# Kernel tuning notes

Hardware: AMD Instinct MI355X
Metric: run time of the kernel (lower is better)

Reference implementation:

```python
import jax, jax.numpy as jnp
import numpy as np

N = 200_000   # fluid particles
DEG = 40      # avg neighbors (2D Wendland support)
E = N * DEG   # edges
SUPPORT = 0.05


def setup_inputs() -> dict:
    key = jax.random.key(0)
    ks = jax.random.split(key, 10)
    i = jnp.sort(jax.random.randint(ks[0], (E,), 0, N))          # target particle per edge
    j = jax.random.randint(ks[1], (E,), 0, N)                    # neighbor particle per edge
    ri = jax.random.uniform(ks[2], (N, 2), dtype=jnp.float32)    # positions (unused in math)
    rj = ri
    dx = SUPPORT * 0.4
    Vi = (0.5 + jax.random.uniform(ks[3], (N,), dtype=jnp.float32)) * dx * dx  # volumes
    Vj = Vi
    d = jax.random.normal(ks[4], (E, 2), dtype=jnp.float32)
    distances = d / jnp.linalg.norm(d, axis=1, keepdims=True)    # unit directions x_ij/|x_ij|
    radialDistances = jax.random.uniform(ks[5], (E,), dtype=jnp.float32)  # q = r/h in [0,1]
    rhoi = 1000.0 * (0.99 + 0.02 * jax.random.uniform(ks[6], (N,), dtype=jnp.float32))
    rhoj = rhoi
    p = 1000.0 * jax.random.normal(ks[7], (N,), dtype=jnp.float32)  # EOS pressure
    return {
        "i": i, "j": j, "ri": ri, "rj": rj, "Vi": Vi, "Vj": Vj,
        "distances": distances, "radialDistances": radialDistances,
        "support": jnp.float32(SUPPORT), "numParticles": N,
        "eps": jnp.float32(SUPPORT * SUPPORT * 0.1),
        "rhoi": rhoi, "rhoj": rhoj, "pi": p, "pj": p,
    }


def _kernel_gradient(q, directions, h):
    # 2D Wendland C2: dW/dq = -20 q (1-q)^3 * (7/pi) / h^3, applied along unit direction
    C = 7.0 / np.pi
    mag = -20.0 * q * (1.0 - q) ** 3 * C / (h ** 3)
    return directions * mag[:, None]  # [E, 2]


def reference(i, j, ri, rj, Vi, Vj, distances, radialDistances, support,
              numParticles, eps, rhoi, rhoj, pi, pj):
    gradW = _kernel_gradient(radialDistances, distances, support)      # [E, 2]
    pij = pi[i] + pj[j]                                                # [E]
    term = (pij * Vj[j])[:, None] * gradW                              # [E, 2]
    acc = jax.ops.segment_sum(term, i, num_segments=numParticles)     # [N, 2]
    return -1.0 / rhoi[:, None] * acc
```

## Files before the change

### kernel.cpp

```cpp
#include <hip/hip_runtime.h>


constexpr int CHUNK = 8;

__global__ void pack_pv(const float* __restrict__ p,
                        const float* __restrict__ V,
                        float2* __restrict__ pv, int N)
{
    int n = blockIdx.x * blockDim.x + threadIdx.x;
    if (n < N) pv[n] = make_float2(p[n], V[n]);
}

__global__ __launch_bounds__(256) void edge_kernel(
    const int*    __restrict__ ei,
    const int*    __restrict__ ej,
    const float*  __restrict__ dirs,
    const float*  __restrict__ qarr,
    const float*  __restrict__ support,
    const float*  __restrict__ p_i,
    const float2* __restrict__ pv,
    float*        __restrict__ acc,
    long long E)
{
    long long t    = blockIdx.x * (long long)blockDim.x + threadIdx.x;
    long long base = t * CHUNK;
    const int lane = threadIdx.x & 63;

    int   cur = -1;
    float ax = 0.0f, ay = 0.0f;

    if (base < E) {
        const float h    = support[0];
        const float coef = -20.0f * (7.0f / 3.14159265358979323846f) / (h * h * h);

        int   ii[CHUNK], jj[CHUNK];
        float qq[CHUNK], dxv[CHUNK], dyv[CHUNK];
        int   nk;

        if (base + CHUNK <= E) {
            const int4*   pi4 = (const int4*)  (ei   + base);
            const int4*   pj4 = (const int4*)  (ej   + base);
            const float4* pq4 = (const float4*)(qarr + base);
            const float4* pd4 = (const float4*)(dirs + 2 * base);
            int4   ia = pi4[0], ib = pi4[1];
            int4   ja = pj4[0], jb = pj4[1];
            float4 qa = pq4[0], qb = pq4[1];
            float4 d0 = pd4[0], d1 = pd4[1], d2 = pd4[2], d3 = pd4[3];
            ii[0]=ia.x; ii[1]=ia.y; ii[2]=ia.z; ii[3]=ia.w;
            ii[4]=ib.x; ii[5]=ib.y; ii[6]=ib.z; ii[7]=ib.w;
            jj[0]=ja.x; jj[1]=ja.y; jj[2]=ja.z; jj[3]=ja.w;
            jj[4]=jb.x; jj[5]=jb.y; jj[6]=jb.z; jj[7]=jb.w;
            qq[0]=qa.x; qq[1]=qa.y; qq[2]=qa.z; qq[3]=qa.w;
            qq[4]=qb.x; qq[5]=qb.y; qq[6]=qb.z; qq[7]=qb.w;
            dxv[0]=d0.x; dyv[0]=d0.y; dxv[1]=d0.z; dyv[1]=d0.w;
            dxv[2]=d1.x; dyv[2]=d1.y; dxv[3]=d1.z; dyv[3]=d1.w;
            dxv[4]=d2.x; dyv[4]=d2.y; dxv[5]=d2.z; dyv[5]=d2.w;
            dxv[6]=d3.x; dyv[6]=d3.y; dxv[7]=d3.z; dyv[7]=d3.w;
            nk = CHUNK;
        } else {
            nk = (int)(E - base);
            #pragma unroll
            for (int k = 0; k < CHUNK; ++k) {
                if (k < nk) {
                    ii[k]  = ei[base + k];
                    jj[k]  = ej[base + k];
                    qq[k]  = qarr[base + k];
                    dxv[k] = dirs[2 * (base + k)];
                    dyv[k] = dirs[2 * (base + k) + 1];
                } else { ii[k] = 0; jj[k] = 0; qq[k] = 0.0f; dxv[k] = 0.0f; dyv[k] = 0.0f; }
            }
        }

        float2 pvv[CHUNK];
        float  piv[CHUNK];
        #pragma unroll
        for (int k = 0; k < CHUNK; ++k) pvv[k] = pv[jj[k]];
        #pragma unroll
        for (int k = 0; k < CHUNK; ++k) piv[k] = p_i[ii[k]];

        float w[CHUNK];
        #pragma unroll
        for (int k = 0; k < CHUNK; ++k) {
            float om = 1.0f - qq[k];
            w[k] = (piv[k] + pvv[k].x) * pvv[k].y * (coef * qq[k] * om * om * om);
        }

        cur = ii[0];
        #pragma unroll
        for (int k = 0; k < CHUNK; ++k) {
            if (k < nk) {
                if (ii[k] != cur) {
                    atomicAdd(&acc[2 * cur],     ax);
                    atomicAdd(&acc[2 * cur + 1], ay);
                    cur = ii[k];
                    ax = 0.0f; ay = 0.0f;
                }
                ax += w[k] * dxv[k];
                ay += w[k] * dyv[k];
            }
        }
    }

    #pragma unroll
    for (int d = 1; d < 64; d <<= 1) {
        int   oc  = __shfl_up(cur, d);
        float oax = __shfl_up(ax,  d);
        float oay = __shfl_up(ay,  d);
        if (lane >= d && oc == cur) { ax += oax; ay += oay; }
    }
    int nxt = __shfl_down(cur, 1);
    if (cur >= 0 && (lane == 63 || nxt != cur)) {
        atomicAdd(&acc[2 * cur],     ax);
        atomicAdd(&acc[2 * cur + 1], ay);
    }
}

__global__ void finalize_kernel(float2* __restrict__ out,
                                const float* __restrict__ rhoi,
                                int N)
{
    int n = blockIdx.x * blockDim.x + threadIdx.x;
    if (n < N) {
        float2 a  = out[n];
        float  sc = -1.0f / rhoi[n];
        out[n] = make_float2(a.x * sc, a.y * sc);
    }
}

extern "C" void kernel_launch(void* const* d_in, const int* in_sizes, int n_in,
                              void* d_out, int out_size, void* d_ws, size_t ws_size,
                              hipStream_t stream)
{
    const int*   ei      = (const int*)  d_in[0];
    const int*   ej      = (const int*)  d_in[1];
    const float* Vj      = (const float*)d_in[5];
    const float* dirs    = (const float*)d_in[6];
    const float* qarr    = (const float*)d_in[7];
    const float* support = (const float*)d_in[8];
    const float* rhoi    = (const float*)d_in[11];
    const float* p_i     = (const float*)d_in[13];
    const float* p_j     = (const float*)d_in[14];

    const long long E = in_sizes[0];
    const int       N = in_sizes[11];

    float* out = (float*)d_out;
    hipMemsetAsync(out, 0, (size_t)N * 2 * sizeof(float), stream);

    const int block = 256;
    float2* pv = (float2*)d_ws;
    pack_pv<<<(N + block - 1) / block, block, 0, stream>>>(p_j, Vj, pv, N);

    const long long nthreads = (E + CHUNK - 1) / CHUNK;
    const int grid = (int)((nthreads + block - 1) / block);
    edge_kernel<<<grid, block, 0, stream>>>(ei, ej, dirs, qarr, support,
                                            p_i, pv, out, E);

    finalize_kernel<<<(N + block - 1) / block, block, 0, stream>>>((float2*)out, rhoi, N);
}
```

Baseline: 70.67 us.

## Fuse memset and finalize into prep kernel, scale atomics by -1/rho in edge kernel

Merges the output zeroing memset and the pack kernel into one prep kernel that also precomputes -1/rho per particle, and removes the finalize pass by scaling each partial sum before its atomicAdd. This cuts two launches and a full read-write pass over the output. It also reorders the loads so the gathered p/V reads issue before the streaming q/direction loads, and adds an occupancy hint of 8 blocks per CU to launch_bounds. In exchange, the edge kernel does an extra gather of -1/rho for every atomic flush.

```diff
diff --git a/kernel.cpp b/kernel.cpp
--- a/kernel.cpp
+++ b/kernel.cpp
@@ -3,15 +3,24 @@
 
 constexpr int CHUNK = 8;
 
-__global__ void pack_pv(const float* __restrict__ p,
-                        const float* __restrict__ V,
-                        float2* __restrict__ pv, int N)
+__global__ __launch_bounds__(256) void prep_kernel(
+    const float* __restrict__ p,
+    const float* __restrict__ V,
+    const float* __restrict__ rho,
+    float2*      __restrict__ pv,
+    float*       __restrict__ nr,
+    float2*      __restrict__ out,
+    int N)
 {
     int n = blockIdx.x * blockDim.x + threadIdx.x;
-    if (n < N) pv[n] = make_float2(p[n], V[n]);
+    if (n < N) {
+        pv[n]  = make_float2(p[n], V[n]);
+        nr[n]  = -1.0f / rho[n];
+        out[n] = make_float2(0.0f, 0.0f);
+    }
 }
 
-__global__ __launch_bounds__(256) void edge_kernel(
+__global__ __launch_bounds__(256, 8) void edge_kernel(
     const int*    __restrict__ ei,
     const int*    __restrict__ ej,
     const float*  __restrict__ dirs,
@@ -19,6 +28,7 @@
     const float*  __restrict__ support,
     const float*  __restrict__ p_i,
     const float2* __restrict__ pv,
+    const float*  __restrict__ nr,
     float*        __restrict__ acc,
     long long E)
 {
@@ -33,41 +43,25 @@
         const float h    = support[0];
         const float coef = -20.0f * (7.0f / 3.14159265358979323846f) / (h * h * h);
 
-        int   ii[CHUNK], jj[CHUNK];
-        float qq[CHUNK], dxv[CHUNK], dyv[CHUNK];
-        int   nk;
+        int ii[CHUNK], jj[CHUNK];
+        int nk;
 
         if (base + CHUNK <= E) {
-            const int4*   pi4 = (const int4*)  (ei   + base);
-            const int4*   pj4 = (const int4*)  (ej   + base);
-            const float4* pq4 = (const float4*)(qarr + base);
-            const float4* pd4 = (const float4*)(dirs + 2 * base);
-            int4   ia = pi4[0], ib = pi4[1];
-            int4   ja = pj4[0], jb = pj4[1];
-            float4 qa = pq4[0], qb = pq4[1];
-            float4 d0 = pd4[0], d1 = pd4[1], d2 = pd4[2], d3 = pd4[3];
+            const int4* pi4 = (const int4*)(ei + base);
+            const int4* pj4 = (const int4*)(ej + base);
+            int4 ia = pi4[0], ib = pi4[1];
+            int4 ja = pj4[0], jb = pj4[1];
             ii[0]=ia.x; ii[1]=ia.y; ii[2]=ia.z; ii[3]=ia.w;
             ii[4]=ib.x; ii[5]=ib.y; ii[6]=ib.z; ii[7]=ib.w;
             jj[0]=ja.x; jj[1]=ja.y; jj[2]=ja.z; jj[3]=ja.w;
             jj[4]=jb.x; jj[5]=jb.y; jj[6]=jb.z; jj[7]=jb.w;
-            qq[0]=qa.x; qq[1]=qa.y; qq[2]=qa.z; qq[3]=qa.w;
-            qq[4]=qb.x; qq[5]=qb.y; qq[6]=qb.z; qq[7]=qb.w;
-            dxv[0]=d0.x; dyv[0]=d0.y; dxv[1]=d0.z; dyv[1]=d0.w;
-            dxv[2]=d1.x; dyv[2]=d1.y; dxv[3]=d1.z; dyv[3]=d1.w;
-            dxv[4]=d2.x; dyv[4]=d2.y; dxv[5]=d2.z; dyv[5]=d2.w;
-            dxv[6]=d3.x; dyv[6]=d3.y; dxv[7]=d3.z; dyv[7]=d3.w;
             nk = CHUNK;
         } else {
             nk = (int)(E - base);
             #pragma unroll
             for (int k = 0; k < CHUNK; ++k) {
-                if (k < nk) {
-                    ii[k]  = ei[base + k];
-                    jj[k]  = ej[base + k];
-                    qq[k]  = qarr[base + k];
-                    dxv[k] = dirs[2 * (base + k)];
-                    dyv[k] = dirs[2 * (base + k) + 1];
-                } else { ii[k] = 0; jj[k] = 0; qq[k] = 0.0f; dxv[k] = 0.0f; dyv[k] = 0.0f; }
+                ii[k] = (k < nk) ? ei[base + k] : 0;
+                jj[k] = (k < nk) ? ej[base + k] : 0;
             }
         }
 
@@ -77,6 +71,27 @@
         for (int k = 0; k < CHUNK; ++k) pvv[k] = pv[jj[k]];
         #pragma unroll
         for (int k = 0; k < CHUNK; ++k) piv[k] = p_i[ii[k]];
+
+        float qq[CHUNK], dxv[CHUNK], dyv[CHUNK];
+        if (base + CHUNK <= E) {
+            const float4* pq4 = (const float4*)(qarr + base);
+            const float4* pd4 = (const float4*)(dirs + 2 * base);
+            float4 qa = pq4[0], qb = pq4[1];
+            float4 d0 = pd4[0], d1 = pd4[1], d2 = pd4[2], d3 = pd4[3];
+            qq[0]=qa.x; qq[1]=qa.y; qq[2]=qa.z; qq[3]=qa.w;
+            qq[4]=qb.x; qq[5]=qb.y; qq[6]=qb.z; qq[7]=qb.w;
+            dxv[0]=d0.x; dyv[0]=d0.y; dxv[1]=d0.z; dyv[1]=d0.w;
+            dxv[2]=d1.x; dyv[2]=d1.y; dxv[3]=d1.z; dyv[3]=d1.w;
+            dxv[4]=d2.x; dyv[4]=d2.y; dxv[5]=d2.z; dyv[5]=d2.w;
+            dxv[6]=d3.x; dyv[6]=d3.y; dxv[7]=d3.z; dyv[7]=d3.w;
+        } else {
+            #pragma unroll
+            for (int k = 0; k < CHUNK; ++k) {
+                qq[k]  = (k < nk) ? qarr[base + k]           : 0.0f;
+                dxv[k] = (k < nk) ? dirs[2 * (base + k)]     : 0.0f;
+                dyv[k] = (k < nk) ? dirs[2 * (base + k) + 1] : 0.0f;
+            }
+        }
 
         float w[CHUNK];
         #pragma unroll
@@ -90,8 +105,9 @@
         for (int k = 0; k < CHUNK; ++k) {
             if (k < nk) {
                 if (ii[k] != cur) {
-                    atomicAdd(&acc[2 * cur],     ax);
-                    atomicAdd(&acc[2 * cur + 1], ay);
+                    float s = nr[cur];
+                    atomicAdd(&acc[2 * cur],     ax * s);
+                    atomicAdd(&acc[2 * cur + 1], ay * s);
                     cur = ii[k];
                     ax = 0.0f; ay = 0.0f;
                 }
@@ -110,20 +126,9 @@
     }
     int nxt = __shfl_down(cur, 1);
     if (cur >= 0 && (lane == 63 || nxt != cur)) {
-        atomicAdd(&acc[2 * cur],     ax);
-        atomicAdd(&acc[2 * cur + 1], ay);
-    }
-}
-
-__global__ void finalize_kernel(float2* __restrict__ out,
-                                const float* __restrict__ rhoi,
-                                int N)
-{
-    int n = blockIdx.x * blockDim.x + threadIdx.x;
-    if (n < N) {
-        float2 a  = out[n];
-        float  sc = -1.0f / rhoi[n];
-        out[n] = make_float2(a.x * sc, a.y * sc);
+        float s = nr[cur];
+        atomicAdd(&acc[2 * cur],     ax * s);
+        atomicAdd(&acc[2 * cur + 1], ay * s);
     }
 }
 
@@ -144,17 +149,16 @@
     const long long E = in_sizes[0];
     const int       N = in_sizes[11];
 
-    float* out = (float*)d_out;
-    hipMemsetAsync(out, 0, (size_t)N * 2 * sizeof(float), stream);
+    float2* pv = (float2*)d_ws;
+    float*  nr = (float*)((char*)d_ws + (size_t)N * sizeof(float2));
 
     const int block = 256;
-    float2* pv = (float2*)d_ws;
-    pack_pv<<<(N + block - 1) / block, block, 0, stream>>>(p_j, Vj, pv, N);
+
+    prep_kernel<<<(N + block - 1) / block, block, 0, stream>>>(
+        p_j, Vj, rhoi, pv, nr, (float2*)d_out, N);
 
     const long long nthreads = (E + CHUNK - 1) / CHUNK;
     const int grid = (int)((nthreads + block - 1) / block);
-    edge_kernel<<<grid, block, 0, stream>>>(ei, ej, dirs, qarr, support,
-                                            p_i, pv, out, E);
-
-    finalize_kernel<<<(N + block - 1) / block, block, 0, stream>>>((float2*)out, rhoi, N);
+    edge_kernel<<<grid, block, 0, stream>>>(
+        ei, ej, dirs, qarr, support, p_i, pv, nr, (float*)d_out, E);
 }
```

Result: slower. 78.24 us (+10.7%).

## Persistent grid-stride edge kernel with software-pipelined index and gather prefetch

Applied to the files above, without the earlier changes.

The edge kernel becomes a persistent grid-stride loop over a fixed grid of 1024 blocks. Each iteration prefetches the next chunk's i/j indices, then issues the next chunk's gathers and streaming loads while the current chunk's wave-level segmented reduction and atomics run. The output memset is folded into the pack kernel, which removes one launch. In exchange the kernel holds more live registers, and a fixed grid may underfill or overfill the GPU.

```diff
diff --git a/kernel.cpp b/kernel.cpp
--- a/kernel.cpp
+++ b/kernel.cpp
@@ -1,17 +1,26 @@
 #include <hip/hip_runtime.h>
 
 
-constexpr int CHUNK = 8;
-
-__global__ void pack_pv(const float* __restrict__ p,
-                        const float* __restrict__ V,
-                        float2* __restrict__ pv, int N)
+constexpr int   CHUNK = 8;
+constexpr int   BLOCK = 256;
+constexpr int   GRID  = 1024;
+constexpr float PI_F  = 3.14159265358979323846f;
+
+__global__ __launch_bounds__(BLOCK) void prep_kernel(
+    const float* __restrict__ p,
+    const float* __restrict__ V,
+    float2*      __restrict__ pv,
+    float2*      __restrict__ out,
+    int N)
 {
     int n = blockIdx.x * blockDim.x + threadIdx.x;
-    if (n < N) pv[n] = make_float2(p[n], V[n]);
-}
-
-__global__ __launch_bounds__(256) void edge_kernel(
+    if (n < N) {
+        pv[n]  = make_float2(p[n], V[n]);
+        out[n] = make_float2(0.0f, 0.0f);
+    }
+}
+
+__global__ __launch_bounds__(BLOCK) void edge_kernel(
     const int*    __restrict__ ei,
     const int*    __restrict__ ej,
     const float*  __restrict__ dirs,
@@ -22,61 +31,86 @@
     float*        __restrict__ acc,
     long long E)
 {
-    long long t    = blockIdx.x * (long long)blockDim.x + threadIdx.x;
-    long long base = t * CHUNK;
+    const long long T   = (long long)GRID * BLOCK;
+    const long long NC  = (E + CHUNK - 1) / CHUNK;
+    long long c   = blockIdx.x * (long long)blockDim.x + threadIdx.x;
     const int lane = threadIdx.x & 63;
-
-    int   cur = -1;
-    float ax = 0.0f, ay = 0.0f;
-
-    if (base < E) {
-        const float h    = support[0];
-        const float coef = -20.0f * (7.0f / 3.14159265358979323846f) / (h * h * h);
-
-        int   ii[CHUNK], jj[CHUNK];
-        float qq[CHUNK], dxv[CHUNK], dyv[CHUNK];
-        int   nk;
-
-        if (base + CHUNK <= E) {
-            const int4*   pi4 = (const int4*)  (ei   + base);
-            const int4*   pj4 = (const int4*)  (ej   + base);
-            const float4* pq4 = (const float4*)(qarr + base);
-            const float4* pd4 = (const float4*)(dirs + 2 * base);
-            int4   ia = pi4[0], ib = pi4[1];
-            int4   ja = pj4[0], jb = pj4[1];
-            float4 qa = pq4[0], qb = pq4[1];
-            float4 d0 = pd4[0], d1 = pd4[1], d2 = pd4[2], d3 = pd4[3];
-            ii[0]=ia.x; ii[1]=ia.y; ii[2]=ia.z; ii[3]=ia.w;
-            ii[4]=ib.x; ii[5]=ib.y; ii[6]=ib.z; ii[7]=ib.w;
-            jj[0]=ja.x; jj[1]=ja.y; jj[2]=ja.z; jj[3]=ja.w;
-            jj[4]=jb.x; jj[5]=jb.y; jj[6]=jb.z; jj[7]=jb.w;
-            qq[0]=qa.x; qq[1]=qa.y; qq[2]=qa.z; qq[3]=qa.w;
-            qq[4]=qb.x; qq[5]=qb.y; qq[6]=qb.z; qq[7]=qb.w;
-            dxv[0]=d0.x; dyv[0]=d0.y; dxv[1]=d0.z; dyv[1]=d0.w;
-            dxv[2]=d1.x; dyv[2]=d1.y; dxv[3]=d1.z; dyv[3]=d1.w;
-            dxv[4]=d2.x; dyv[4]=d2.y; dxv[5]=d2.z; dyv[5]=d2.w;
-            dxv[6]=d3.x; dyv[6]=d3.y; dxv[7]=d3.z; dyv[7]=d3.w;
-            nk = CHUNK;
-        } else {
-            nk = (int)(E - base);
-            #pragma unroll
-            for (int k = 0; k < CHUNK; ++k) {
-                if (k < nk) {
-                    ii[k]  = ei[base + k];
-                    jj[k]  = ej[base + k];
-                    qq[k]  = qarr[base + k];
-                    dxv[k] = dirs[2 * (base + k)];
-                    dyv[k] = dirs[2 * (base + k) + 1];
-                } else { ii[k] = 0; jj[k] = 0; qq[k] = 0.0f; dxv[k] = 0.0f; dyv[k] = 0.0f; }
-            }
-        }
-
-        float2 pvv[CHUNK];
-        float  piv[CHUNK];
-        #pragma unroll
-        for (int k = 0; k < CHUNK; ++k) pvv[k] = pv[jj[k]];
-        #pragma unroll
-        for (int k = 0; k < CHUNK; ++k) piv[k] = p_i[ii[k]];
+    long long wfc = c - lane;
+
+    if (wfc >= NC) return;
+
+    const float h    = support[0];
+    const float coef = -20.0f * (7.0f / PI_F) / (h * h * h);
+
+    int    iiA[CHUNK], jjA[CHUNK];
+    int    iiB[CHUNK], jjB[CHUNK];
+    float2 pvv[CHUNK];
+    float  piv[CHUNK], qq[CHUNK], dxv[CHUNK], dyv[CHUNK];
+
+#define LOAD_IDX(cc, ii, jj)                                                   \
+    do {                                                                       \
+        long long b_ = (cc) * CHUNK;                                           \
+        if ((cc) < NC && b_ + CHUNK <= E) {                                    \
+            const int4* pi4_ = (const int4*)(ei + b_);                         \
+            const int4* pj4_ = (const int4*)(ej + b_);                         \
+            int4 ia_ = pi4_[0], ib_ = pi4_[1];                                 \
+            int4 ja_ = pj4_[0], jb_ = pj4_[1];                                 \
+            ii[0]=ia_.x; ii[1]=ia_.y; ii[2]=ia_.z; ii[3]=ia_.w;                \
+            ii[4]=ib_.x; ii[5]=ib_.y; ii[6]=ib_.z; ii[7]=ib_.w;                \
+            jj[0]=ja_.x; jj[1]=ja_.y; jj[2]=ja_.z; jj[3]=ja_.w;                \
+            jj[4]=jb_.x; jj[5]=jb_.y; jj[6]=jb_.z; jj[7]=jb_.w;                \
+        } else {                                                               \
+            _Pragma("unroll")                                                  \
+            for (int k_ = 0; k_ < CHUNK; ++k_) {                               \
+                long long e_ = b_ + k_;                                        \
+                bool ok_ = ((cc) < NC) && (e_ < E);                            \
+                ii[k_] = ok_ ? ei[e_] : -1;                                    \
+                jj[k_] = ok_ ? ej[e_] : 0;                                     \
+            }                                                                  \
+        }                                                                      \
+    } while (0)
+
+#define LOAD_GS(cc, ii, jj)                                                    \
+    do {                                                                       \
+        long long b_ = (cc) * CHUNK;                                           \
+        _Pragma("unroll")                                                      \
+        for (int k_ = 0; k_ < CHUNK; ++k_) pvv[k_] = pv[jj[k_]];               \
+        _Pragma("unroll")                                                      \
+        for (int k_ = 0; k_ < CHUNK; ++k_) {                                   \
+            int i_ = ii[k_] < 0 ? 0 : ii[k_];                                  \
+            piv[k_] = p_i[i_];                                                 \
+        }                                                                      \
+        if ((cc) < NC && b_ + CHUNK <= E) {                                    \
+            const float4* pq4_ = (const float4*)(qarr + b_);                   \
+            const float4* pd4_ = (const float4*)(dirs + 2 * b_);               \
+            float4 qa_ = pq4_[0], qb_ = pq4_[1];                               \
+            float4 d0_ = pd4_[0], d1_ = pd4_[1], d2_ = pd4_[2], d3_ = pd4_[3]; \
+            qq[0]=qa_.x; qq[1]=qa_.y; qq[2]=qa_.z; qq[3]=qa_.w;                \
+            qq[4]=qb_.x; qq[5]=qb_.y; qq[6]=qb_.z; qq[7]=qb_.w;                \
+            dxv[0]=d0_.x; dyv[0]=d0_.y; dxv[1]=d0_.z; dyv[1]=d0_.w;            \
+            dxv[2]=d1_.x; dyv[2]=d1_.y; dxv[3]=d1_.z; dyv[3]=d1_.w;            \
+            dxv[4]=d2_.x; dyv[4]=d2_.y; dxv[5]=d2_.z; dyv[5]=d2_.w;            \
+            dxv[6]=d3_.x; dyv[6]=d3_.y; dxv[7]=d3_.z; dyv[7]=d3_.w;            \
+        } else {                                                               \
+            _Pragma("unroll")                                                  \
+            for (int k_ = 0; k_ < CHUNK; ++k_) {                               \
+                long long e_ = b_ + k_;                                        \
+                bool ok_ = ((cc) < NC) && (e_ < E);                            \
+                qq[k_]  = ok_ ? qarr[e_]           : 0.0f;                     \
+                dxv[k_] = ok_ ? dirs[2 * e_]       : 0.0f;                     \
+                dyv[k_] = ok_ ? dirs[2 * e_ + 1]   : 0.0f;                     \
+            }                                                                  \
+        }                                                                      \
+    } while (0)
+
+    LOAD_IDX(c, iiA, jjA);
+    LOAD_GS(c, iiA, jjA);
+
+    for (;;) {
+        long long cn = c + T;
+        bool have_next = (wfc + T) < NC;
+
+        if (have_next) LOAD_IDX(cn, iiB, jjB);
 
         float w[CHUNK];
         #pragma unroll
@@ -85,39 +119,52 @@
             w[k] = (piv[k] + pvv[k].x) * pvv[k].y * (coef * qq[k] * om * om * om);
         }
 
-        cur = ii[0];
+        int   cur = iiA[0];
+        float ax = 0.0f, ay = 0.0f;
         #pragma unroll
         for (int k = 0; k < CHUNK; ++k) {
-            if (k < nk) {
-                if (ii[k] != cur) {
+            if (iiA[k] != cur) {
+                if (cur >= 0) {
                     atomicAdd(&acc[2 * cur],     ax);
                     atomicAdd(&acc[2 * cur + 1], ay);
-                    cur = ii[k];
-                    ax = 0.0f; ay = 0.0f;
                 }
-                ax += w[k] * dxv[k];
-                ay += w[k] * dyv[k];
+                cur = iiA[k];
+                ax = 0.0f; ay = 0.0f;
             }
-        }
+            ax += w[k] * dxv[k];
+            ay += w[k] * dyv[k];
+        }
+
+        if (have_next) LOAD_GS(cn, iiB, jjB);
+
+        #pragma unroll
+        for (int d = 1; d < 64; d <<= 1) {
+            int   oc  = __shfl_up(cur, d);
+            float oax = __shfl_up(ax,  d);
+            float oay = __shfl_up(ay,  d);
+            if (lane >= d && oc == cur) { ax += oax; ay += oay; }
+        }
+        int nxt = __shfl_down(cur, 1);
+        if (cur >= 0 && (lane == 63 || nxt != cur)) {
+            atomicAdd(&acc[2 * cur],     ax);
+            atomicAdd(&acc[2 * cur + 1], ay);
+        }
+
+        if (!have_next) break;
+        #pragma unroll
+        for (int k = 0; k < CHUNK; ++k) { iiA[k] = iiB[k]; jjA[k] = jjB[k]; }
+        c = cn;
+        wfc += T;
     }
 
-    #pragma unroll
-    for (int d = 1; d < 64; d <<= 1) {
-        int   oc  = __shfl_up(cur, d);
-        float oax = __shfl_up(ax,  d);
-        float oay = __shfl_up(ay,  d);
-        if (lane >= d && oc == cur) { ax += oax; ay += oay; }
-    }
-    int nxt = __shfl_down(cur, 1);
-    if (cur >= 0 && (lane == 63 || nxt != cur)) {
-        atomicAdd(&acc[2 * cur],     ax);
-        atomicAdd(&acc[2 * cur + 1], ay);
-    }
-}
-
-__global__ void finalize_kernel(float2* __restrict__ out,
-                                const float* __restrict__ rhoi,
-                                int N)
+#undef LOAD_IDX
+#undef LOAD_GS
+}
+
+__global__ __launch_bounds__(BLOCK) void finalize_kernel(
+    float2* __restrict__ out,
+    const float* __restrict__ rhoi,
+    int N)
 {
     int n = blockIdx.x * blockDim.x + threadIdx.x;
     if (n < N) {
@@ -144,17 +191,14 @@
     const long long E = in_sizes[0];
     const int       N = in_sizes[11];
 
-    float* out = (float*)d_out;
-    hipMemsetAsync(out, 0, (size_t)N * 2 * sizeof(float), stream);
-
-    const int block = 256;
     float2* pv = (float2*)d_ws;
-    pack_pv<<<(N + block - 1) / block, block, 0, stream>>>(p_j, Vj, pv, N);
-
-    const long long nthreads = (E + CHUNK - 1) / CHUNK;
-    const int grid = (int)((nthreads + block - 1) / block);
-    edge_kernel<<<grid, block, 0, stream>>>(ei, ej, dirs, qarr, support,
-                                            p_i, pv, out, E);
-
-    finalize_kernel<<<(N + block - 1) / block, block, 0, stream>>>((float2*)out, rhoi, N);
-}
+
+    prep_kernel<<<(N + BLOCK - 1) / BLOCK, BLOCK, 0, stream>>>(
+        p_j, Vj, pv, (float2*)d_out, N);
+
+    edge_kernel<<<GRID, BLOCK, 0, stream>>>(
+        ei, ej, dirs, qarr, support, p_i, pv, (float*)d_out, E);
+
+    finalize_kernel<<<(N + BLOCK - 1) / BLOCK, BLOCK, 0, stream>>>(
+        (float2*)d_out, rhoi, N);
+}
```

Result: faster. 67.98 us (-3.8%).
